# Performance work log

Hardware: AMD Instinct MI355X
Metric: run time of the kernel (lower is better)

## Reference

```python
import jax, jax.numpy as jnp
import numpy as np

B, T, E, H = 4, 2048, 1024, 16
D = E // H  # head_size = 64

def setup_inputs() -> dict:
    key = jax.random.key(0)
    ks = jax.random.split(key, 8)
    s = 1.0 / np.sqrt(E)
    inp = {
        'k': jax.random.normal(ks[0], (B, T, E), jnp.float32),
        'q': jax.random.normal(ks[1], (B, T, E), jnp.float32),
        'v': jax.random.normal(ks[2], (B, T, E), jnp.float32),
        'mask': jnp.triu(jnp.ones((T, T), jnp.bool_), k=1),  # True above diagonal -> masked
        # per-head projection weights stacked: [H, E, D], no bias (bias=False)
        'Wk': jax.random.uniform(ks[3], (H, E, D), jnp.float32, -s, s),
        'Wq': jax.random.uniform(ks[4], (H, E, D), jnp.float32, -s, s),
        'Wv': jax.random.uniform(ks[5], (H, E, D), jnp.float32, -s, s),
        # output projection (bias=True default)
        'Wp': jax.random.uniform(ks[6], (E, E), jnp.float32, -s, s),
        'bp': jax.random.uniform(ks[7], (E,), jnp.float32, -s, s),
    }
    return inp

def reference(k, q, v, mask, Wk, Wq, Wv, Wp, bp):
    # per-head projections (bias=False Linears), batched over heads
    xk = jnp.einsum('bte,hed->bhtd', k, Wk)
    xq = jnp.einsum('bte,hed->bhtd', q, Wq)
    xv = jnp.einsum('bte,hed->bhtd', v, Wv)
    # NOTE: original scales by sqrt(C) where C = embed_size (input dim), not head_size
    wei = jnp.einsum('bhtd,bhsd->bhts', xq, xk) / jnp.sqrt(jnp.asarray(E, xq.dtype))
    wei = jnp.where(mask, -jnp.inf, wei)  # masked_fill(mask, -inf)
    wei = jax.nn.softmax(wei, axis=-1)
    out = jnp.einsum('bhts,bhsd->bhtd', wei, xv)
    out = out.transpose(0, 2, 1, 3).reshape(B, T, E)  # concat heads on last dim
    return out @ Wp.T + bp
```

## Files before the change

### kernel.cpp

```cpp
#include <hip/hip_runtime.h>
#include <cstdint>
#include <cstddef>


#define B_ 4
#define T_ 2048
#define E_ 1024
#define H_ 16
#define D_ 64
#define MROWS 8192
#define MK    8388608
#define SCALE_LOG2E 0.045084220027780106f

typedef unsigned short u16;
typedef unsigned int   u32;
typedef __attribute__((ext_vector_type(4))) float  f32x4;
typedef __attribute__((ext_vector_type(4))) u32    u32x4;
typedef __attribute__((ext_vector_type(8))) u16    u16x8;
typedef __attribute__((ext_vector_type(8))) __bf16 bf16x8;

typedef __attribute__((address_space(1))) void gvoid_t;
typedef __attribute__((address_space(3))) void lvoid_t;

__device__ __forceinline__ void async_load16(const void* g, void* l) {
  __builtin_amdgcn_global_load_lds((gvoid_t*)(uintptr_t)g, (lvoid_t*)l, 16, 0, 0);
}

__device__ __forceinline__ u16 f2bf(float f) {
  u32 u = __builtin_bit_cast(u32, f);
  u = (u + 0x7FFFu + ((u >> 16) & 1u)) >> 16;
  return (u16)u;
}

__device__ __forceinline__ u16 f2bf_hw(float f) {
  return __builtin_bit_cast(u16, (__bf16)f);
}

__device__ __forceinline__ float fast_exp2(float x) {
#if __has_builtin(__builtin_amdgcn_exp2f)
  return __builtin_amdgcn_exp2f(x);
#else
  return exp2f(x);
#endif
}

__device__ __forceinline__ bf16x8 ldfrag(const u16* p) {
  u32x4 t = *(const u32x4*)p;
  return __builtin_bit_cast(bf16x8, t);
}

__device__ __forceinline__ bf16x8 ldfrag_g(const u16* p) {
  u32x4 t = *(const u32x4*)p;
  return __builtin_bit_cast(bf16x8, t);
}

__device__ __forceinline__ f32x4 mfma_bf16(bf16x8 a, bf16x8 b, f32x4 c) {
  return __builtin_amdgcn_mfma_f32_16x16x32_bf16(a, b, c, 0, 0, 0);
}

__global__ __launch_bounds__(256) void cast_qkv_kernel(
    const float* __restrict__ q, const float* __restrict__ k,
    const float* __restrict__ v, u16* __restrict__ dst) {
  const int z = blockIdx.y;
  const float* src = (z == 0) ? q : (z == 1) ? k : v;
  const float sc = (z == 0) ? SCALE_LOG2E : 1.0f;
  u16* out = dst + (size_t)z * MK;
  size_t i0 = ((size_t)blockIdx.x * 256 + threadIdx.x) * 8;
  float4 a = *(const float4*)(src + i0);
  float4 b = *(const float4*)(src + i0 + 4);
  u16x8 o;
  o[0] = f2bf_hw(a.x * sc); o[1] = f2bf_hw(a.y * sc);
  o[2] = f2bf_hw(a.z * sc); o[3] = f2bf_hw(a.w * sc);
  o[4] = f2bf_hw(b.x * sc); o[5] = f2bf_hw(b.y * sc);
  o[6] = f2bf_hw(b.z * sc); o[7] = f2bf_hw(b.w * sc);
  *(u16x8*)(out + i0) = o;
}

__global__ __launch_bounds__(256) void prep_weights_kernel(
    const float* __restrict__ Wq, const float* __restrict__ Wk,
    const float* __restrict__ Wv, const float* __restrict__ Wp,
    u16* __restrict__ dstW, u16* __restrict__ dstWp) {
  const int z = blockIdx.y;
  const int t = blockIdx.x * 256 + threadIdx.x;
  if (z == 3) { dstWp[t] = f2bf(Wp[t]); return; }
  const float* W = (z == 0) ? Wq : (z == 1) ? Wk : Wv;
  const int j = t >> 10, e = t & 1023;
  const int h = j >> 6, d = j & 63;
  dstW[(size_t)z * (E_ * E_) + t] = f2bf(W[h * (E_ * D_) + e * D_ + d]);
}

template <int FINAL>
__global__ __launch_bounds__(256) void gemm_bt_kernel(
    const u16* __restrict__ Abase, const u16* __restrict__ Btbase,
    u16* __restrict__ Cb, float* __restrict__ Cf,
    const float* __restrict__ bias) {
  constexpr int Md = 8192, Nd = 1024, Kd = 1024;
  __shared__ __align__(16) u16 As[128 * 64];
  __shared__ __align__(16) u16 Bs[128 * 64];
  const int tid = threadIdx.x;
  const int wave = tid >> 6, lane = tid & 63;
  const int l16 = lane & 15, quad = lane >> 4;
  const int z = blockIdx.z;
  const u16* A  = Abase  + (size_t)z * Md * Kd;
  const u16* Bt = Btbase + (size_t)z * Nd * Kd;
  const int tm = blockIdx.x * 128, tn = blockIdx.y * 128;
  const int wm = (wave >> 1) * 64, wn = (wave & 1) * 64;

  f32x4 acc[4][4];
#pragma unroll
  for (int i = 0; i < 4; ++i)
#pragma unroll
    for (int j = 0; j < 4; ++j) acc[i][j] = f32x4{0.f, 0.f, 0.f, 0.f};

  const int r8  = lane >> 3;
  const int csw = (lane & 7) ^ r8;
  const u16* Ag = A  + (size_t)(tm + wave * 8 + r8) * Kd + csw * 8;
  const u16* Bg = Bt + (size_t)(tn + wave * 8 + r8) * Kd + csw * 8;
  char* AsB = (char*)&As[0];
  char* BsB = (char*)&Bs[0];
  const int dst0 = wave * 1024;

  const int xr = l16 & 7;

  for (int kt = 0; kt < Kd / 64; ++kt) {
#pragma unroll
    for (int i = 0; i < 4; ++i)
      async_load16(Ag + (size_t)i * 32 * Kd, AsB + i * 4096 + dst0);
#pragma unroll
    for (int i = 0; i < 4; ++i)
      async_load16(Bg + (size_t)i * 32 * Kd, BsB + i * 4096 + dst0);
    Ag += 64; Bg += 64;
    __syncthreads();
#pragma unroll
    for (int ks = 0; ks < 2; ++ks) {
      bf16x8 af[4], bfr[4];
#pragma unroll
      for (int i = 0; i < 4; ++i) {
        const int ch = (ks * 4 + quad) ^ xr;
        af[i]  = ldfrag(&As[(wm + i * 16 + l16) * 64 + ch * 8]);
        bfr[i] = ldfrag(&Bs[(wn + i * 16 + l16) * 64 + ch * 8]);
      }
#pragma unroll
      for (int mi = 0; mi < 4; ++mi)
#pragma unroll
        for (int ni = 0; ni < 4; ++ni)
          acc[mi][ni] = mfma_bf16(af[mi], bfr[ni], acc[mi][ni]);
    }
    __syncthreads();
  }

  if (FINAL) {
    float bv[4];
#pragma unroll
    for (int ni = 0; ni < 4; ++ni) bv[ni] = bias[tn + wn + ni * 16 + l16];
#pragma unroll
    for (int mi = 0; mi < 4; ++mi)
#pragma unroll
      for (int r = 0; r < 4; ++r) {
        const int row = tm + wm + mi * 16 + quad * 4 + r;
        float* cp = Cf + (size_t)row * Nd + tn + wn;
#pragma unroll
        for (int ni = 0; ni < 4; ++ni)
          cp[ni * 16 + l16] = acc[mi][ni][r] + bv[ni];
      }
  } else {
    u16* C = Cb + (size_t)z * Md * Nd;
#pragma unroll
    for (int mi = 0; mi < 4; ++mi)
#pragma unroll
      for (int r = 0; r < 4; ++r) {
        const int row = tm + wm + mi * 16 + quad * 4 + r;
        u16* cp = C + (size_t)row * Nd + tn + wn;
#pragma unroll
        for (int ni = 0; ni < 4; ++ni)
          cp[ni * 16 + l16] = f2bf_hw(acc[mi][ni][r]);
      }
  }
}

__global__ __launch_bounds__(256, 3) void attn_kernel(
    const u16* __restrict__ Xq, const u16* __restrict__ Xk,
    const u16* __restrict__ Xv, u16* __restrict__ Xo) {
  const int qt = 15 - blockIdx.y;
  const int bh = blockIdx.x;
  const int b = bh >> 4, h = bh & 15;
  const int tid = threadIdx.x, wave = tid >> 6, lane = tid & 63;
  const int l16 = lane & 15, quad = lane >> 4;

  __shared__ __align__(16) u16 Ks[2 * 4096];
  __shared__ __align__(16) u16 Vts[2 * 4096];
  __shared__ __align__(16) u16 Ps[128 * 64];

  const size_t base = (size_t)b * T_ * E_ + h * 64;
  const u16* Qp = Xq + base + (size_t)qt * 128 * E_;
  const u16* Kp = Xk + base;
  const u16* Vp = Xv + base;
  char* KsB = (char*)&Ks[0];

  const int r8  = lane >> 3;
  const int csw = (lane & 7) ^ r8;
  const int xr  = l16 & 7;

  auto stageK = [&](int kt, int buf) {
#pragma unroll
    for (int i = 0; i < 2; ++i) {
      const int c = wave + i * 4;
      async_load16(Kp + (size_t)(kt * 64 + c * 8 + r8) * E_ + csw * 8,
                   KsB + buf * 8192 + c * 1024);
    }
  };
  auto loadV = [&](int kt, u32x4* vreg) {
#pragma unroll
    for (int i = 0; i < 2; ++i) {
      const int dseg = wave + i * 4;
      vreg[i] = *(const u32x4*)(Vp + (size_t)(kt * 64 + lane) * E_ + dseg * 8);
    }
  };
  auto writeV = [&](int buf, const u32x4* vreg) {
#pragma unroll
    for (int i = 0; i < 2; ++i) {
      const int dseg = wave + i * 4;
      union { u32x4 v; u16 s[8]; } t; t.v = vreg[i];
#pragma unroll
      for (int ii = 0; ii < 8; ++ii)
        Vts[buf * 4096 + (dseg * 8 + ii) * 64 + ((r8 ^ ii) * 8) + (lane & 7)] =
            t.s[ii];
    }
  };

  bf16x8 qf[2][2];
#pragma unroll
  for (int mi = 0; mi < 2; ++mi)
#pragma unroll
    for (int ks = 0; ks < 2; ++ks)
      qf[mi][ks] = ldfrag_g(Qp + (size_t)(wave * 32 + mi * 16 + l16) * E_ +
                            ks * 32 + quad * 8);

  u16x8 ones_u;
#pragma unroll
  for (int i = 0; i < 8; ++i) ones_u[i] = 0x3F80;
  const bf16x8 ones = __builtin_bit_cast(bf16x8, ones_u);

  f32x4 o_acc[2][4];
#pragma unroll
  for (int mi = 0; mi < 2; ++mi)
#pragma unroll
    for (int di = 0; di < 4; ++di) o_acc[mi][di] = f32x4{0.f, 0.f, 0.f, 0.f};
  f32x4 lrow[2] = {f32x4{0.f, 0.f, 0.f, 0.f}, f32x4{0.f, 0.f, 0.f, 0.f}};

  {
    u32x4 vreg[2];
    stageK(0, 0);
    loadV(0, vreg);
    writeV(0, vreg);
  }

  const int kt_end = 2 * qt + 1;
  for (int kt = 0; kt <= kt_end; ++kt) {
    const int buf = kt & 1;
    __syncthreads();

    bf16x8 kf[4][2];
#pragma unroll
    for (int ni = 0; ni < 4; ++ni)
#pragma unroll
      for (int ks = 0; ks < 2; ++ks)
        kf[ni][ks] = ldfrag(&Ks[buf * 4096 + (ni * 16 + l16) * 64 +
                                (((ks * 4 + quad) ^ xr) * 8)]);

    f32x4 sa[2][4];
    __builtin_amdgcn_s_setprio(1);
#pragma unroll
    for (int mi = 0; mi < 2; ++mi)
#pragma unroll
      for (int ni = 0; ni < 4; ++ni) {
        f32x4 s = f32x4{0.f, 0.f, 0.f, 0.f};
        s = mfma_bf16(qf[mi][0], kf[ni][0], s);
        s = mfma_bf16(qf[mi][1], kf[ni][1], s);
        sa[mi][ni] = s;
      }
    __builtin_amdgcn_s_setprio(0);

    u32x4 vreg[2];
    const bool have_next = (kt < kt_end);
    if (have_next) {
      stageK(kt + 1, buf ^ 1);
      loadV(kt + 1, vreg);
    }

    if (kt >= 2 * qt) {
#pragma unroll
      for (int mi = 0; mi < 2; ++mi) {
        const int grow0 = qt * 128 + wave * 32 + mi * 16 + quad * 4;
#pragma unroll
        for (int ni = 0; ni < 4; ++ni) {
          const int gcol = kt * 64 + ni * 16 + l16;
#pragma unroll
          for (int r = 0; r < 4; ++r)
            if (gcol > grow0 + r) sa[mi][ni][r] = -INFINITY;
        }
      }
    }

#pragma unroll
    for (int mi = 0; mi < 2; ++mi) {
#pragma unroll
      for (int ni = 0; ni < 4; ++ni)
#pragma unroll
        for (int r = 0; r < 4; ++r)
          sa[mi][ni][r] = fast_exp2(sa[mi][ni][r]);
#pragma unroll
      for (int r = 0; r < 4; ++r) {
        const int row = wave * 32 + mi * 16 + quad * 4 + r;
        const int rx = (quad * 4 + r) & 7;
#pragma unroll
        for (int ni = 0; ni < 4; ++ni)
          Ps[row * 64 + (((ni * 2 + (l16 >> 3)) ^ rx) * 8) + (l16 & 7)] =
              f2bf_hw(sa[mi][ni][r]);
      }
    }

    if (have_next) writeV(buf ^ 1, vreg);

    bf16x8 pf[2][2], vf[4][2];
#pragma unroll
    for (int mi = 0; mi < 2; ++mi)
#pragma unroll
      for (int ks = 0; ks < 2; ++ks)
        pf[mi][ks] = ldfrag(&Ps[(wave * 32 + mi * 16 + l16) * 64 +
                                (((ks * 4 + quad) ^ xr) * 8)]);
#pragma unroll
    for (int di = 0; di < 4; ++di)
#pragma unroll
      for (int ks = 0; ks < 2; ++ks)
        vf[di][ks] = ldfrag(&Vts[buf * 4096 + (di * 16 + l16) * 64 +
                                 (((ks * 4 + quad) ^ xr) * 8)]);
    __builtin_amdgcn_s_setprio(1);
#pragma unroll
    for (int mi = 0; mi < 2; ++mi) {
      lrow[mi] = mfma_bf16(pf[mi][0], ones, lrow[mi]);
      lrow[mi] = mfma_bf16(pf[mi][1], ones, lrow[mi]);
#pragma unroll
      for (int di = 0; di < 4; ++di) {
        o_acc[mi][di] = mfma_bf16(pf[mi][0], vf[di][0], o_acc[mi][di]);
        o_acc[mi][di] = mfma_bf16(pf[mi][1], vf[di][1], o_acc[mi][di]);
      }
    }
    __builtin_amdgcn_s_setprio(0);
  }

  u16* Op = Xo + base + (size_t)qt * 128 * E_;
#pragma unroll
  for (int mi = 0; mi < 2; ++mi)
#pragma unroll
    for (int r = 0; r < 4; ++r) {
      const float inv = 1.0f / lrow[mi][r];
      const int row = wave * 32 + mi * 16 + quad * 4 + r;
#pragma unroll
      for (int di = 0; di < 4; ++di)
        Op[(size_t)row * E_ + di * 16 + l16] = f2bf_hw(o_acc[mi][di][r] * inv);
    }
}

extern "C" void kernel_launch(void* const* d_in, const int* in_sizes, int n_in,
                              void* d_out, int out_size, void* d_ws, size_t ws_size,
                              hipStream_t stream) {
  const float* k_in = (const float*)d_in[0];
  const float* q_in = (const float*)d_in[1];
  const float* v_in = (const float*)d_in[2];
  const float* Wk = (const float*)d_in[4];
  const float* Wq = (const float*)d_in[5];
  const float* Wv = (const float*)d_in[6];
  const float* Wp = (const float*)d_in[7];
  const float* bp = (const float*)d_in[8];
  float* out = (float*)d_out;

  char* ws = (char*)d_ws;
  u16* qkvb = (u16*)ws;
  u16* Wt   = (u16*)(ws + 50331648);
  u16* Wpb  = (u16*)(ws + 56623104);
  u16* X    = (u16*)(ws + 58720256);
  u16* Xo   = (u16*)ws;

  cast_qkv_kernel<<<dim3(4096, 3), 256, 0, stream>>>(q_in, k_in, v_in, qkvb);
  prep_weights_kernel<<<dim3(4096, 4), 256, 0, stream>>>(Wq, Wk, Wv, Wp, Wt, Wpb);
  gemm_bt_kernel<0><<<dim3(64, 8, 3), 256, 0, stream>>>(qkvb, Wt, X, nullptr, nullptr);
  attn_kernel<<<dim3(64, 16), 256, 0, stream>>>(X, X + (size_t)MK, X + (size_t)2 * MK, Xo);
  gemm_bt_kernel<1><<<dim3(64, 8, 1), 256, 0, stream>>>(Xo, Wpb, nullptr, out, bp);
}
```

Before: 315.6 us.

## Keep attention probabilities in registers via transposed QK MFMA and ds_bpermute

Computes S^T by swapping the MFMA operands, so each lane holds consecutive key columns for one query row. The bf16 probabilities are packed and redistributed with ds_bpermute straight into the A-operand layout of the PV MFMA, removing the shared-memory P tile along with its stores and loads. Freeing that LDS allows launch bounds to rise from 3 to 4 blocks per SIMD. The cost is extra cross-lane permute instructions and selects, and the tighter register budget could cause spills.

```diff
diff --git a/kernel.cpp b/kernel.cpp
--- a/kernel.cpp
+++ b/kernel.cpp
@@ -36,12 +36,20 @@
   return __builtin_bit_cast(u16, (__bf16)f);
 }
 
+__device__ __forceinline__ u32 packbf(float lo, float hi) {
+  return (u32)f2bf_hw(lo) | ((u32)f2bf_hw(hi) << 16);
+}
+
 __device__ __forceinline__ float fast_exp2(float x) {
 #if __has_builtin(__builtin_amdgcn_exp2f)
   return __builtin_amdgcn_exp2f(x);
 #else
   return exp2f(x);
 #endif
+}
+
+__device__ __forceinline__ u32 bperm(int addr, u32 v) {
+  return (u32)__builtin_amdgcn_ds_bpermute(addr, (int)v);
 }
 
 __device__ __forceinline__ bf16x8 ldfrag(const u16* p) {
@@ -178,7 +186,7 @@
   }
 }
 
-__global__ __launch_bounds__(256, 3) void attn_kernel(
+__global__ __launch_bounds__(256, 4) void attn_kernel(
     const u16* __restrict__ Xq, const u16* __restrict__ Xk,
     const u16* __restrict__ Xv, u16* __restrict__ Xo) {
   const int qt = 15 - blockIdx.y;
@@ -189,7 +197,6 @@
 
   __shared__ __align__(16) u16 Ks[2 * 4096];
   __shared__ __align__(16) u16 Vts[2 * 4096];
-  __shared__ __align__(16) u16 Ps[128 * 64];
 
   const size_t base = (size_t)b * T_ * E_ + h * 64;
   const u16* Qp = Xq + base + (size_t)qt * 128 * E_;
@@ -200,6 +207,10 @@
   const int r8  = lane >> 3;
   const int csw = (lane & 7) ^ r8;
   const int xr  = l16 & 7;
+
+  const int addr0 = (l16 + 16 * ((2 * quad) & 3)) * 4;
+  const int addr1 = (l16 + 16 * ((2 * quad + 1) & 3)) * 4;
+  const bool hiq = quad >= 2;
 
   auto stageK = [&](int kt, int buf) {
 #pragma unroll
@@ -275,8 +286,8 @@
 #pragma unroll
       for (int ni = 0; ni < 4; ++ni) {
         f32x4 s = f32x4{0.f, 0.f, 0.f, 0.f};
-        s = mfma_bf16(qf[mi][0], kf[ni][0], s);
-        s = mfma_bf16(qf[mi][1], kf[ni][1], s);
+        s = mfma_bf16(kf[ni][0], qf[mi][0], s);
+        s = mfma_bf16(kf[ni][1], qf[mi][1], s);
         sa[mi][ni] = s;
       }
     __builtin_amdgcn_s_setprio(0);
@@ -291,17 +302,18 @@
     if (kt >= 2 * qt) {
 #pragma unroll
       for (int mi = 0; mi < 2; ++mi) {
-        const int grow0 = qt * 128 + wave * 32 + mi * 16 + quad * 4;
+        const int qrow = qt * 128 + wave * 32 + mi * 16 + l16;
 #pragma unroll
         for (int ni = 0; ni < 4; ++ni) {
-          const int gcol = kt * 64 + ni * 16 + l16;
+          const int kcol0 = kt * 64 + ni * 16 + quad * 4;
 #pragma unroll
           for (int r = 0; r < 4; ++r)
-            if (gcol > grow0 + r) sa[mi][ni][r] = -INFINITY;
+            if (kcol0 + r > qrow) sa[mi][ni][r] = -INFINITY;
         }
       }
     }
 
+    bf16x8 pa[2][2];
 #pragma unroll
     for (int mi = 0; mi < 2; ++mi) {
 #pragma unroll
@@ -309,26 +321,28 @@
 #pragma unroll
         for (int r = 0; r < 4; ++r)
           sa[mi][ni][r] = fast_exp2(sa[mi][ni][r]);
-#pragma unroll
-      for (int r = 0; r < 4; ++r) {
-        const int row = wave * 32 + mi * 16 + quad * 4 + r;
-        const int rx = (quad * 4 + r) & 7;
-#pragma unroll
-        for (int ni = 0; ni < 4; ++ni)
-          Ps[row * 64 + (((ni * 2 + (l16 >> 3)) ^ rx) * 8) + (l16 & 7)] =
-              f2bf_hw(sa[mi][ni][r]);
+      u32 upk[8];
+#pragma unroll
+      for (int ni = 0; ni < 4; ++ni)
+#pragma unroll
+        for (int hh = 0; hh < 2; ++hh)
+          upk[ni * 2 + hh] =
+              packbf(sa[mi][ni][2 * hh], sa[mi][ni][2 * hh + 1]);
+#pragma unroll
+      for (int ks = 0; ks < 2; ++ks) {
+        const int nlo = 2 * ks * 2, nhi = (2 * ks + 1) * 2;
+        u32 a0 = bperm(addr0, upk[nlo + 0]), b0 = bperm(addr0, upk[nhi + 0]);
+        u32 a1 = bperm(addr0, upk[nlo + 1]), b1 = bperm(addr0, upk[nhi + 1]);
+        u32 a2 = bperm(addr1, upk[nlo + 0]), b2 = bperm(addr1, upk[nhi + 0]);
+        u32 a3 = bperm(addr1, upk[nlo + 1]), b3 = bperm(addr1, upk[nhi + 1]);
+        u32x4 t = {hiq ? b0 : a0, hiq ? b1 : a1, hiq ? b2 : a2, hiq ? b3 : a3};
+        pa[mi][ks] = __builtin_bit_cast(bf16x8, t);
       }
     }
 
     if (have_next) writeV(buf ^ 1, vreg);
 
-    bf16x8 pf[2][2], vf[4][2];
-#pragma unroll
-    for (int mi = 0; mi < 2; ++mi)
-#pragma unroll
-      for (int ks = 0; ks < 2; ++ks)
-        pf[mi][ks] = ldfrag(&Ps[(wave * 32 + mi * 16 + l16) * 64 +
-                                (((ks * 4 + quad) ^ xr) * 8)]);
+    bf16x8 vf[4][2];
 #pragma unroll
     for (int di = 0; di < 4; ++di)
 #pragma unroll
@@ -338,12 +352,12 @@
     __builtin_amdgcn_s_setprio(1);
 #pragma unroll
     for (int mi = 0; mi < 2; ++mi) {
-      lrow[mi] = mfma_bf16(pf[mi][0], ones, lrow[mi]);
-      lrow[mi] = mfma_bf16(pf[mi][1], ones, lrow[mi]);
+      lrow[mi] = mfma_bf16(pa[mi][0], ones, lrow[mi]);
+      lrow[mi] = mfma_bf16(pa[mi][1], ones, lrow[mi]);
 #pragma unroll
       for (int di = 0; di < 4; ++di) {
-        o_acc[mi][di] = mfma_bf16(pf[mi][0], vf[di][0], o_acc[mi][di]);
-        o_acc[mi][di] = mfma_bf16(pf[mi][1], vf[di][1], o_acc[mi][di]);
+        o_acc[mi][di] = mfma_bf16(pa[mi][0], vf[di][0], o_acc[mi][di]);
+        o_acc[mi][di] = mfma_bf16(pa[mi][1], vf[di][1], o_acc[mi][di]);
       }
     }
     __builtin_amdgcn_s_setprio(0);
```

Result: slower. 328.3 us (+4.0%).
